# Kernel optimization log

Measured on AMD Instinct MI355X. Metric: run time of the kernel, lower is better.

Reference implementation:

```python
import jax, jax.numpy as jnp
from jax import lax
import numpy as np

N = 1024           # num_nodes
E = 32768          # edges per hop adjacency (avg degree 32)
EMB, HID, REP = 128, 64, 32
PATH_LENGTHS = (2, 3)


def _conv2d(x, w, b, pad):
    y = lax.conv_general_dilated(x, w, (1, 1), [(pad, pad), (pad, pad)],
                                 dimension_numbers=('NCHW', 'OIHW', 'NCHW'))
    return y + b[None, :, None, None]


def _tconv2d(x, w, b):
    # ConvTranspose2d(kernel=2, stride=2, pad=0) == conv with lhs_dilation=2, pad=1 (out = 2*in)
    y = lax.conv_general_dilated(x, w, (1, 1), [(1, 1), (1, 1)],
                                 lhs_dilation=(2, 2),
                                 dimension_numbers=('NCHW', 'OIHW', 'NCHW'))
    return y + b[None, :, None, None]


def _maxpool2(x):
    return lax.reduce_window(x, -jnp.inf, lax.max, (1, 1, 2, 2), (1, 1, 2, 2), 'VALID')


def _att_block(a, p):
    # ConvEncoder: conv->pool->conv->pool->tconv->tconv, relu/relu/relu/sigmoid
    h = jax.nn.relu(_conv2d(a, p[0], p[1], 1))
    h = _maxpool2(h)
    h = jax.nn.relu(_conv2d(h, p[2], p[3], 2))
    h = _maxpool2(h)
    h = jax.nn.relu(_tconv2d(h, p[4], p[5]))
    return jax.nn.sigmoid(_tconv2d(h, p[6], p[7]))


def _dense_gcn_norm(A):
    # add_remaining_self_loops(fill=1) + D^{-1/2} A D^{-1/2}; deg = row-sum (scatter_add over row)
    A = A + jnp.diag(jnp.where(jnp.diagonal(A) == 0, 1.0, 0.0).astype(A.dtype))
    deg = A.sum(axis=1)
    safe = jnp.where(deg > 0, deg, 1.0)
    dinv = jnp.where(deg > 0, lax.rsqrt(safe), 0.0)
    return dinv[:, None] * A * dinv[None, :]


def _edges_to_dense(e):
    # torch.sparse.FloatTensor(idx, ones).to_dense() sums duplicate edges
    return jnp.zeros((N, N), jnp.float32).at[e[0], e[1]].add(1.0)


def _path_transform(adjs, p):
    # adjs: [L, N, N] dense per-hop adjacencies of one meta-path
    att = _att_block(adjs[None], p)[0][:, :N, :N]
    attended = adjs * att
    M = jnp.eye(N, dtype=adjs.dtype)
    for i in range(adjs.shape[0]):  # fixed small loop over hops
        M = _dense_gcn_norm(M @ attended[i])
    return M


def _forward(x, p0, p1, w1, bias1, w2, bias2, e00, e01, e10, e11, e12):
    A0 = jnp.stack([_edges_to_dense(e00), _edges_to_dense(e01)])
    A1 = jnp.stack([_edges_to_dense(e10), _edges_to_dense(e11), _edges_to_dense(e12)])
    M0 = _path_transform(A0, p0)
    M1 = _path_transform(A1, p1)
    A = jnp.maximum(M0, M1)  # coalesce(op='max') over union; values are >= 0
    An = _dense_gcn_norm(A)  # GCNConv internal normalization (same for both layers)
    h = jax.nn.relu(An @ (x @ w1) + bias1)
    # dropout inactive (eval mode)
    return An @ (h @ w2) + bias2


def setup_inputs():
    key = jax.random.key(0)
    ks = iter(jax.random.split(key, 40))
    d = {}
    d['x'] = jax.random.normal(next(ks), (N, EMB), jnp.float32)
    d['mp0_e0'] = jax.random.randint(next(ks), (2, E), 0, N)
    d['mp0_e1'] = jax.random.randint(next(ks), (2, E), 0, N)
    d['mp1_e0'] = jax.random.randint(next(ks), (2, E), 0, N)
    d['mp1_e1'] = jax.random.randint(next(ks), (2, E), 0, N)
    d['mp1_e2'] = jax.random.randint(next(ks), (2, E), 0, N)
    for bi, L in enumerate(PATH_LENGTHS):
        pre = 'b%d_' % bi
        d[pre + 'c1w'] = jax.random.normal(next(ks), (16, L, 3, 3), jnp.float32) * 0.1
        d[pre + 'c1b'] = jnp.zeros((16,), jnp.float32)
        d[pre + 'c2w'] = jax.random.normal(next(ks), (4, 16, 3, 3), jnp.float32) * 0.1
        d[pre + 'c2b'] = jnp.zeros((4,), jnp.float32)
        d[pre + 't1w'] = jax.random.normal(next(ks), (16, 4, 2, 2), jnp.float32) * 0.1
        d[pre + 't1b'] = jnp.zeros((16,), jnp.float32)
        d[pre + 't2w'] = jax.random.normal(next(ks), (L, 16, 2, 2), jnp.float32) * 0.1
        d[pre + 't2b'] = jnp.zeros((L,), jnp.float32)
    d['w1'] = jax.random.normal(next(ks), (EMB, HID), jnp.float32) * (1.0 / np.sqrt(EMB)).astype(np.float32)
    d['bias1'] = jnp.zeros((HID,), jnp.float32)
    d['w2'] = jax.random.normal(next(ks), (HID, REP), jnp.float32) * (1.0 / np.sqrt(HID)).astype(np.float32)
    d['bias2'] = jnp.zeros((REP,), jnp.float32)
    return d


def reference(x, mp0_e0, mp0_e1, mp1_e0, mp1_e1, mp1_e2,
              b0_c1w, b0_c1b, b0_c2w, b0_c2b, b0_t1w, b0_t1b, b0_t2w, b0_t2b,
              b1_c1w, b1_c1b, b1_c2w, b1_c2b, b1_t1w, b1_t1b, b1_t2w, b1_t2b,
              w1, bias1, w2, bias2):
    p0 = (b0_c1w, b0_c1b, b0_c2w, b0_c2b, b0_t1w, b0_t1b, b0_t2w, b0_t2b)
    p1 = (b1_c1w, b1_c1b, b1_c2w, b1_c2b, b1_t1w, b1_t1b, b1_t2w, b1_t2b)
    return _forward(x, p0, p1, w1, bias1, w2, bias2,
                    mp0_e0, mp0_e1, mp1_e0, mp1_e1, mp1_e2)
```

## Files before the change

kernel.cpp:

```cpp
#include <hip/hip_runtime.h>
#include <math.h>

#define N 1024
#define NN (N*N)
#define NE 32768

#define OFF_A    ((size_t)0)
#define OFF_H10  ((size_t)(5*NN))
#define OFF_M0   ((size_t)(5*NN))
#define OFF_CSR  ((size_t)(7*NN))
#define OFF_BT   ((size_t)(9*NN))
#define OFF_M1   ((size_t)(10*NN))
#define OFF_AN   ((size_t)(11*NN))
#define OFF_H20  ((size_t)(13*NN))
#define OFF_H21  (OFF_H20 + 264196)
#define OFF_SC   (OFF_H21 + 264196)
#define SC_D0a 0
#define SC_F0a 1024
#define SC_D1a 2048
#define SC_F1a 3072
#define SC_D0b 4096
#define SC_F0b 5120
#define SC_D1b 6144
#define SC_F1b 7168
#define SC_D1c 8192
#define SC_F1c 9216
#define SC_D2  10240
#define SC_F2  11264
#define OFF_XW1  (OFF_SC + 12288)
#define OFF_HB   (OFF_XW1 + 65536)
#define OFF_HW2  (OFF_HB + 65536)

#define CSR_STRIDE 96
#define CSRF (1024 * CSR_STRIDE)
#define CSC_MAXT 80

__global__ void k_scatter5(const int* __restrict__ e0, const int* __restrict__ e1,
                           const int* __restrict__ e2, const int* __restrict__ e3,
                           const int* __restrict__ e4, float* __restrict__ A) {
  int g = blockIdx.x * 256 + threadIdx.x;
  int seg = g >> 15;
  int k = g & 32767;
  const int* e = (seg == 0) ? e0 : (seg == 1) ? e1 : (seg == 2) ? e2 : (seg == 3) ? e3 : e4;
  atomicAdd(&A[(size_t)seg * NN + (size_t)e[k] * N + e[NE + k]], 1.0f);
}

template<int L>
__device__ __forceinline__ void conv1_body(const float* __restrict__ A,
    const float* __restrict__ W, const float* __restrict__ Bn, float* __restrict__ out) {
  __shared__ float sIn[L][34][35];
  __shared__ float sW[16 * L * 9];
  __shared__ float sB[16];
  int tid = threadIdx.y * 16 + threadIdx.x;
  for (int i = tid; i < 16 * L * 9; i += 256) sW[i] = W[i];
  if (tid < 16) sB[tid] = Bn[tid];
  const int x0 = blockIdx.x * 32 - 1;
  const int y0 = blockIdx.y * 32 - 1;
  for (int idx = tid; idx < L * 34 * 34; idx += 256) {
    int l = idx / (34 * 34);
    int rem = idx - l * 34 * 34;
    int r = rem / 34, c = rem - r * 34;
    int iy = y0 + r, ix = x0 + c;
    sIn[l][r][c] = (iy >= 0 && iy < N && ix >= 0 && ix < N) ? A[(size_t)l * NN + (size_t)iy * N + ix] : 0.f;
  }
  __syncthreads();
  const int tx = threadIdx.x, ty = threadIdx.y;
  float p[L][4][4];
  #pragma unroll
  for (int l = 0; l < L; ++l)
    #pragma unroll
    for (int r = 0; r < 4; ++r)
      #pragma unroll
      for (int c = 0; c < 4; ++c)
        p[l][r][c] = sIn[l][2 * ty + r][2 * tx + c];
  const int ox = blockIdx.x * 16 + tx;
  const int oy = blockIdx.y * 16 + ty;
  for (int oc = 0; oc < 16; ++oc) {
    float wr[L * 9];
    #pragma unroll
    for (int t = 0; t < L * 9; ++t) wr[t] = sW[oc * L * 9 + t];
    float m = -1e30f;
    #pragma unroll
    for (int dy = 0; dy < 2; ++dy)
      #pragma unroll
      for (int dx = 0; dx < 2; ++dx) {
        float s = 0.f;
        #pragma unroll
        for (int l = 0; l < L; ++l)
          #pragma unroll
          for (int ky = 0; ky < 3; ++ky)
            #pragma unroll
            for (int kx = 0; kx < 3; ++kx)
              s = fmaf(p[l][dy + ky][dx + kx], wr[l * 9 + ky * 3 + kx], s);
        m = fmaxf(m, s);
      }
    out[(size_t)oc * 512 * 512 + (size_t)oy * 512 + ox] = fmaxf(m + sB[oc], 0.f);
  }
}

__global__ __launch_bounds__(256) void k_conv1_both(const float* __restrict__ Ab,
    const float* __restrict__ W0, const float* __restrict__ b0,
    const float* __restrict__ W1, const float* __restrict__ b1, float* __restrict__ H1b) {
  if (blockIdx.z == 0) conv1_body<2>(Ab, W0, b0, H1b);
  else                 conv1_body<3>(Ab + 2 * NN, W1, b1, H1b + 4 * NN);
}

__global__ __launch_bounds__(256) void k_conv2_both(const float* __restrict__ H1b,
    const float* __restrict__ W0, const float* __restrict__ b0,
    const float* __restrict__ W1, const float* __restrict__ b1,
    float* __restrict__ H2_0, float* __restrict__ H2_1) {
  const int z = blockIdx.z;
  const float* in = H1b + (size_t)z * 4 * NN;
  const float* W  = z ? W1 : W0;
  const float* Bn = z ? b1 : b0;
  float* out = z ? H2_1 : H2_0;
  __shared__ float sIn[2][4][36][37];
  __shared__ float sW[4 * 16 * 9];
  __shared__ float sB[4];
  int tid = threadIdx.y * 16 + threadIdx.x;
  for (int i = tid; i < 4 * 16 * 9; i += 256) sW[i] = W[i];
  if (tid < 4) sB[tid] = Bn[tid];
  const int x0 = blockIdx.x * 32 - 2;
  const int y0 = blockIdx.y * 32 - 2;
  const int tx = threadIdx.x, ty = threadIdx.y;

  auto stage = [&](int g, int buf) {
    for (int idx = tid; idx < 4 * 36 * 36; idx += 256) {
      int icl = idx / 1296;
      int rem = idx - icl * 1296;
      int r = rem / 36, c = rem - r * 36;
      int iy = y0 + r, ix = x0 + c;
      sIn[buf][icl][r][c] = (iy >= 0 && iy < 512 && ix >= 0 && ix < 512)
                            ? in[(size_t)(4 * g + icl) * 262144 + (size_t)iy * 512 + ix] : 0.f;
    }
  };

  float acc[4][2][2];
  #pragma unroll
  for (int oc = 0; oc < 4; ++oc)
    #pragma unroll
    for (int dy = 0; dy < 2; ++dy)
      #pragma unroll
      for (int dx = 0; dx < 2; ++dx) acc[oc][dy][dx] = 0.f;

  stage(0, 0);
  for (int g = 0; g < 4; ++g) {
    __syncthreads();
    if (g < 3) stage(g + 1, (g + 1) & 1);
    const int buf = g & 1;
    #pragma unroll
    for (int icl = 0; icl < 4; ++icl) {
      float p[4][4];
      #pragma unroll
      for (int r = 0; r < 4; ++r)
        #pragma unroll
        for (int c = 0; c < 4; ++c) p[r][c] = sIn[buf][icl][2 * ty + r][2 * tx + c];
      #pragma unroll
      for (int oc = 0; oc < 4; ++oc)
        #pragma unroll
        for (int ky = 0; ky < 3; ++ky)
          #pragma unroll
          for (int kx = 0; kx < 3; ++kx) {
            float w = sW[oc * 144 + (4 * g + icl) * 9 + ky * 3 + kx];
            #pragma unroll
            for (int dy = 0; dy < 2; ++dy)
              #pragma unroll
              for (int dx = 0; dx < 2; ++dx)
                acc[oc][dy][dx] = fmaf(p[dy + ky][dx + kx], w, acc[oc][dy][dx]);
          }
    }
  }
  const int ox = blockIdx.x * 16 + tx;
  const int oy = blockIdx.y * 16 + ty;
  if (ox < 257 && oy < 257) {
    #pragma unroll
    for (int oc = 0; oc < 4; ++oc) {
      float m = fmaxf(fmaxf(acc[oc][0][0], acc[oc][0][1]), fmaxf(acc[oc][1][0], acc[oc][1][1]));
      out[(size_t)oc * 66049 + (size_t)oy * 257 + ox] = fmaxf(m + sB[oc], 0.f);
    }
  }
}

__global__ __launch_bounds__(256) void k_tc_both(
    const float* __restrict__ H2_0, const float* __restrict__ H2_1,
    const float* __restrict__ t1w0, const float* __restrict__ t1b0,
    const float* __restrict__ t2w0, const float* __restrict__ t2b0,
    const float* __restrict__ t1w1, const float* __restrict__ t1b1,
    const float* __restrict__ t2w1, const float* __restrict__ t2b1,
    float* __restrict__ Ab) {
  const int z = blockIdx.z;
  const int L = 2 + z;
  const float* in  = z ? H2_1 : H2_0;
  const float* W1p = z ? t1w1 : t1w0;
  const float* B1p = z ? t1b1 : t1b0;
  const float* W2p = z ? t2w1 : t2w0;
  const float* B2p = z ? t2b1 : t2b0;
  float* A = Ab + (size_t)z * 2 * NN;
  __shared__ float sW1[256], sB1[16], sW2[192], sB2[3];
  int tid = threadIdx.y * 16 + threadIdx.x;
  sW1[tid] = W1p[tid];
  if (tid < 16) sB1[tid] = B1p[tid];
  for (int i = tid; i < L * 64; i += 256) sW2[i] = W2p[i];
  if (tid < L) sB2[tid] = B2p[tid];
  __syncthreads();
  const int n = blockIdx.x * 16 + threadIdx.x;
  const int m = blockIdx.y * 16 + threadIdx.y;
  const int p = m >> 1, q = n >> 1;
  const int f1y = 1 - (m & 1), f1x = 1 - (n & 1);
  float vin[4];
  #pragma unroll
  for (int ci = 0; ci < 4; ++ci) vin[ci] = in[(size_t)ci * 66049 + (size_t)p * 257 + q];
  float v[16];
  #pragma unroll
  for (int c = 0; c < 16; ++c) {
    float s = sB1[c];
    #pragma unroll
    for (int ci = 0; ci < 4; ++ci)
      s = fmaf(vin[ci], sW1[c * 16 + ci * 4 + f1y * 2 + f1x], s);
    v[c] = fmaxf(s, 0.f);
  }
  for (int l = 0; l < L; ++l) {
    #pragma unroll
    for (int dy = 0; dy < 2; ++dy)
      #pragma unroll
      for (int dx = 0; dx < 2; ++dx) {
        float s = sB2[l];
        #pragma unroll
        for (int c = 0; c < 16; ++c)
          s = fmaf(v[c], sW2[l * 64 + c * 4 + (1 - dy) * 2 + (1 - dx)], s);
        float sg = 1.f / (1.f + expf(-s));
        size_t idx = (size_t)l * NN + (size_t)(2 * m + dy) * N + (2 * n + dx);
        A[idx] *= sg;
      }
  }
}

__global__ __launch_bounds__(256) void k_extract(const float* __restrict__ Ab,
    int* __restrict__ gcol, float* __restrict__ gval, int* __restrict__ gcnt,
    int* __restrict__ crowT, float* __restrict__ cvalT, int* __restrict__ ccnt,
    float* __restrict__ D0a, float* __restrict__ F0a,
    float* __restrict__ D1a, float* __restrict__ F1a) {
  const int row = blockIdx.x;
  const int y = blockIdx.y;
  const float* base = Ab + (size_t)y * NN + (size_t)row * N;
  __shared__ int cnt;
  __shared__ float sdiag;
  __shared__ float red[4];
  if (threadIdx.x == 0) cnt = 0;
  __syncthreads();
  const int j4 = threadIdx.x;
  float4 v = ((const float4*)base)[j4];
  if (j4 == (row >> 2)) sdiag = ((const float*)&v)[row & 3];
  if (y == 4) {
    #pragma unroll
    for (int t = 0; t < 4; ++t) {
      float x = ((const float*)&v)[t];
      if (x != 0.f) {
        int j = 4 * j4 + t;
        int p = atomicAdd(&ccnt[j], 1);
        if (p < CSC_MAXT) { crowT[p * 1024 + j] = row; cvalT[p * 1024 + j] = x; }
      }
    }
    return;
  }
  const size_t rb = ((size_t)y * 1024 + row) * CSR_STRIDE;
  #pragma unroll
  for (int t = 0; t < 4; ++t) {
    float x = ((const float*)&v)[t];
    if (x != 0.f) {
      int p = atomicAdd(&cnt, 1);
      if (p < CSR_STRIDE) { gcol[rb + p] = 4 * j4 + t; gval[rb + p] = x; }
    }
  }
  float s = v.x + v.y + v.z + v.w;
  #pragma unroll
  for (int o = 32; o > 0; o >>= 1) s += __shfl_down(s, o, 64);
  if ((threadIdx.x & 63) == 0) red[threadIdx.x >> 6] = s;
  __syncthreads();
  if (threadIdx.x == 0) {
    gcnt[(size_t)y * 1024 + row] = (cnt < CSR_STRIDE) ? cnt : CSR_STRIDE;
    if (y == 0 || y == 2) {
      float tot = red[0] + red[1] + red[2] + red[3];
      float fl = (sdiag == 0.f) ? 1.f : 0.f;
      float deg = tot + fl;
      float* D = (y == 0) ? D0a : D1a;
      float* F = (y == 0) ? F0a : F1a;
      D[row] = (deg > 0.f) ? (1.f / sqrtf(deg)) : 0.f;
      F[row] = fl;
    }
  }
}

__global__ __launch_bounds__(256) void k_spmm(
    const int* __restrict__ gcol, const float* __restrict__ gval, const int* __restrict__ gcnt,
    const float* __restrict__ D0a, const float* __restrict__ F0a,
    const float* __restrict__ D1a, const float* __restrict__ F1a,
    float* __restrict__ M0, float* __restrict__ BT,
    float* __restrict__ D0b, float* __restrict__ F0b,
    float* __restrict__ D1b, float* __restrict__ F1b) {
  const int row = blockIdx.x;
  const int y = blockIdx.y;
  const int lm = y * 2, rm = y * 2 + 1;
  const float* Da = y ? D1a : D0a;
  const float* Fa = y ? F1a : F0a;
  __shared__ __align__(16) float acc[1024];
  __shared__ int lcol[112];
  __shared__ float lw[112];
  __shared__ int lrc[112];
  __shared__ int cl;
  __shared__ float red[4];
  __shared__ float sdiag;
  ((float4*)acc)[threadIdx.x] = make_float4(0.f, 0.f, 0.f, 0.f);
  const float di = Da[row];
  const int cnt_l = gcnt[(size_t)lm * 1024 + row];
  const size_t lb = ((size_t)lm * 1024 + row) * CSR_STRIDE;
  if (threadIdx.x < cnt_l) {
    int k = gcol[lb + threadIdx.x];
    lcol[threadIdx.x] = k;
    lw[threadIdx.x] = di * gval[lb + threadIdx.x] * Da[k];
    lrc[threadIdx.x] = gcnt[(size_t)rm * 1024 + k];
  }
  if (threadIdx.x == 0) {
    int c = cnt_l;
    if (Fa[row] != 0.f) {
      lcol[c] = row; lw[c] = di * di; lrc[c] = gcnt[(size_t)rm * 1024 + row]; ++c;
    }
    cl = c;
  }
  __syncthreads();
  const int sub = threadIdx.x >> 5, lane = threadIdx.x & 31;
  const int cle = cl;
  for (int e = sub; e < cle; e += 8) {
    const int k = lcol[e];
    const float w = lw[e];
    const int rc = lrc[e];
    const size_t rbv = ((size_t)rm * 1024 + k) * CSR_STRIDE;
    for (int t = lane; t < rc; t += 32)
      atomicAdd(&acc[gcol[rbv + t]], w * gval[rbv + t]);
  }
  __syncthreads();
  float4 o = ((const float4*)acc)[threadIdx.x];
  float* C = y ? BT : M0;
  ((float4*)(C + (size_t)row * N))[threadIdx.x] = o;
  if (threadIdx.x == (row >> 2)) sdiag = ((const float*)&o)[row & 3];
  float s = o.x + o.y + o.z + o.w;
  #pragma unroll
  for (int off = 32; off > 0; off >>= 1) s += __shfl_down(s, off, 64);
  if ((threadIdx.x & 63) == 0) red[threadIdx.x >> 6] = s;
  __syncthreads();
  if (threadIdx.x == 0) {
    float tot = red[0] + red[1] + red[2] + red[3];
    float fl = (sdiag == 0.f) ? 1.f : 0.f;
    float deg = tot + fl;
    float* D = y ? D1b : D0b;
    float* F = y ? F1b : F0b;
    D[row] = (deg > 0.f) ? (1.f / sqrtf(deg)) : 0.f;
    F[row] = fl;
  }
}

__global__ __launch_bounds__(256) void k_spmm2(const float* __restrict__ BT,
    const float* __restrict__ D1b, const float* __restrict__ F1b,
    const int* __restrict__ crowT, const float* __restrict__ cvalT, const int* __restrict__ ccnt,
    float* __restrict__ M1, float* __restrict__ D1c, float* __restrict__ F1c) {
  const int row = blockIdx.x;
  __shared__ __align__(16) float bt[1024];
  __shared__ float red[4];
  __shared__ float sdiag;
  const int tid = threadIdx.x;
  {
    float4 b = ((const float4*)(BT + (size_t)row * N))[tid];
    float4 d = ((const float4*)D1b)[tid];
    ((float4*)bt)[tid] = make_float4(b.x * d.x, b.y * d.y, b.z * d.z, b.w * d.w);
  }
  __syncthreads();
  if (tid == 0) bt[row] += F1b[row] * D1b[row];
  __syncthreads();
  const int j0 = tid << 2;
  int4 cn = *(const int4*)&ccnt[j0];
  cn.x = min(cn.x, CSC_MAXT); cn.y = min(cn.y, CSC_MAXT);
  cn.z = min(cn.z, CSC_MAXT); cn.w = min(cn.w, CSC_MAXT);
  const int tmax = max(max(cn.x, cn.y), max(cn.z, cn.w));
  float4 o = make_float4(0.f, 0.f, 0.f, 0.f);
  for (int t = 0; t < tmax; ++t) {
    const int4   r = *(const int4*)&crowT[t * 1024 + j0];
    const float4 v = *(const float4*)&cvalT[t * 1024 + j0];
    if (t < cn.x) o.x = fmaf(bt[r.x], v.x, o.x);
    if (t < cn.y) o.y = fmaf(bt[r.y], v.y, o.y);
    if (t < cn.z) o.z = fmaf(bt[r.z], v.z, o.z);
    if (t < cn.w) o.w = fmaf(bt[r.w], v.w, o.w);
  }
  const float dr = D1b[row];
  o.x *= dr; o.y *= dr; o.z *= dr; o.w *= dr;
  ((float4*)(M1 + (size_t)row * N))[tid] = o;
  if (tid == (row >> 2)) sdiag = ((const float*)&o)[row & 3];
  float s = o.x + o.y + o.z + o.w;
  #pragma unroll
  for (int off = 32; off > 0; off >>= 1) s += __shfl_down(s, off, 64);
  if ((tid & 63) == 0) red[tid >> 6] = s;
  __syncthreads();
  if (tid == 0) {
    float tot = red[0] + red[1] + red[2] + red[3];
    float fl = (sdiag == 0.f) ? 1.f : 0.f;
    float deg = tot + fl;
    D1c[row] = (deg > 0.f) ? (1.f / sqrtf(deg)) : 0.f;
    F1c[row] = fl;
  }
}

__global__ __launch_bounds__(256) void k_maxdeg(const float* __restrict__ M0,
    const float* __restrict__ d0, const float* __restrict__ f0,
    const float* __restrict__ M1, const float* __restrict__ d1, const float* __restrict__ f1,
    float* __restrict__ Aout, float* __restrict__ dinv2, float* __restrict__ dflg2) {
  const int row = blockIdx.x;
  const int j4 = threadIdx.x;
  const float r0 = d0[row], r1 = d1[row];
  const float fl0 = f0[row], fl1 = f1[row];
  float4 a = ((const float4*)(M0 + (size_t)row * N))[j4];
  float4 b = ((const float4*)(M1 + (size_t)row * N))[j4];
  const float4 c0 = ((const float4*)d0)[j4];
  const float4 c1 = ((const float4*)d1)[j4];
  int d = row - 4 * j4;
  if ((unsigned)d < 4u) { ((float*)&a)[d] += fl0; ((float*)&b)[d] += fl1; }
  float4 o;
  o.x = fmaxf(a.x * r0 * c0.x, b.x * r1 * c1.x);
  o.y = fmaxf(a.y * r0 * c0.y, b.y * r1 * c1.y);
  o.z = fmaxf(a.z * r0 * c0.z, b.z * r1 * c1.z);
  o.w = fmaxf(a.w * r0 * c0.w, b.w * r1 * c1.w);
  ((float4*)(Aout + (size_t)row * N))[j4] = o;
  __shared__ float sdiag;
  if ((unsigned)d < 4u) sdiag = ((float*)&o)[d];
  float s = o.x + o.y + o.z + o.w;
  #pragma unroll
  for (int off = 32; off > 0; off >>= 1) s += __shfl_down(s, off, 64);
  __shared__ float red[4];
  if ((threadIdx.x & 63) == 0) red[threadIdx.x >> 6] = s;
  __syncthreads();
  if (threadIdx.x == 0) {
    float tot = red[0] + red[1] + red[2] + red[3];
    float fl = (sdiag == 0.0f) ? 1.0f : 0.0f;
    float deg = tot + fl;
    dinv2[row] = (deg > 0.0f) ? (1.0f / sqrtf(deg)) : 0.0f;
    dflg2[row] = fl;
  }
}

template<int K, int NCOL, bool BIAS, bool RELU>
__global__ void k_mm_small(const float* __restrict__ A, const float* __restrict__ B,
                           const float* __restrict__ bias, float* __restrict__ out) {
  const int j = threadIdx.x;
  const int i = blockIdx.x * blockDim.y + threadIdx.y;
  const float* ar = A + (size_t)i * K;
  float acc = 0.f;
  #pragma unroll 8
  for (int k = 0; k < K; ++k) acc = fmaf(ar[k], B[(size_t)k * NCOL + j], acc);
  if (BIAS) acc += bias[j];
  if (RELU) acc = fmaxf(acc, 0.f);
  out[(size_t)i * NCOL + j] = acc;
}

template<int NCOL, bool RELU>
__global__ void k_an_mm(const float* __restrict__ BT, const float* __restrict__ dinv,
                        const float* __restrict__ dflg, const float* __restrict__ Bm,
                        const float* __restrict__ bias, float* __restrict__ out) {
  const int j = threadIdx.x;
  const int i = blockIdx.x * blockDim.y + threadIdx.y;
  const float di = dinv[i];
  const float* ar = BT + (size_t)i * N;
  float acc = 0.f;
  for (int k = 0; k < N; k += 4) {
    float4 a4 = *(const float4*)&ar[k];
    float4 d4 = *(const float4*)&dinv[k];
    acc = fmaf(a4.x * d4.x, Bm[(size_t)(k + 0) * NCOL + j], acc);
    acc = fmaf(a4.y * d4.y, Bm[(size_t)(k + 1) * NCOL + j], acc);
    acc = fmaf(a4.z * d4.z, Bm[(size_t)(k + 2) * NCOL + j], acc);
    acc = fmaf(a4.w * d4.w, Bm[(size_t)(k + 3) * NCOL + j], acc);
  }
  acc = fmaf(dflg[i] * dinv[i], Bm[(size_t)i * NCOL + j], acc);
  acc = fmaf(di, acc, bias[j]);
  if (RELU) acc = fmaxf(acc, 0.f);
  out[(size_t)i * NCOL + j] = acc;
}

extern "C" void kernel_launch(void* const* d_in, const int* in_sizes, int n_in,
                              void* d_out, int out_size, void* d_ws, size_t ws_size,
                              hipStream_t stream) {
  const float* x     = (const float*)d_in[0];
  const float* w1    = (const float*)d_in[22];
  const float* bias1 = (const float*)d_in[23];
  const float* w2    = (const float*)d_in[24];
  const float* bias2 = (const float*)d_in[25];
  float* out = (float*)d_out;
  float* ws  = (float*)d_ws;

  float* A    = ws + OFF_A;
  float* H1   = ws + OFF_H10;
  float* M0   = ws + OFF_M0;
  float* BT   = ws + OFF_BT;
  float* M1   = ws + OFF_M1;
  float* AN   = ws + OFF_AN;
  float* H2_0 = ws + OFF_H20;
  float* H2_1 = ws + OFF_H21;
  int*   gcol  = (int*)(ws + OFF_CSR);
  float* gval  = ws + OFF_CSR + (size_t)4 * CSRF;
  int*   gcnt  = (int*)(ws + OFF_CSR + (size_t)8 * CSRF);
  int*   crowT = (int*)(ws + OFF_CSR + (size_t)8 * CSRF + 4096);
  float* cvalT = ws + OFF_CSR + (size_t)8 * CSRF + 4096 + CSC_MAXT * 1024;
  int*   ccnt  = (int*)(ws + OFF_CSR + (size_t)8 * CSRF + 4096 + (size_t)2 * CSC_MAXT * 1024);
  float* SC   = ws + OFF_SC;
  float *D0a = SC + SC_D0a, *F0a = SC + SC_F0a, *D1a = SC + SC_D1a, *F1a = SC + SC_F1a;
  float *D0b = SC + SC_D0b, *F0b = SC + SC_F0b, *D1b = SC + SC_D1b, *F1b = SC + SC_F1b;
  float *D1c = SC + SC_D1c, *F1c = SC + SC_F1c, *D2 = SC + SC_D2, *F2 = SC + SC_F2;
  float* XW1 = ws + OFF_XW1;
  float* HB  = ws + OFF_HB;
  float* HW2 = ws + OFF_HW2;

  hipMemsetAsync(A, 0, (size_t)5 * NN * sizeof(float), stream);

  dim3 b256(256), b16(16, 16);
  k_mm_small<128, 64, false, false><<<256, dim3(64, 4), 0, stream>>>(x, w1, nullptr, XW1);

  k_scatter5<<<640, b256, 0, stream>>>((const int*)d_in[1], (const int*)d_in[2],
                                       (const int*)d_in[3], (const int*)d_in[4],
                                       (const int*)d_in[5], A);

  k_conv1_both<<<dim3(32, 32, 2), b16, 0, stream>>>(A,
      (const float*)d_in[6], (const float*)d_in[7],
      (const float*)d_in[14], (const float*)d_in[15], H1);
  k_conv2_both<<<dim3(17, 17, 2), b16, 0, stream>>>(H1,
      (const float*)d_in[8], (const float*)d_in[9],
      (const float*)d_in[16], (const float*)d_in[17], H2_0, H2_1);
  k_tc_both<<<dim3(32, 32, 2), b16, 0, stream>>>(H2_0, H2_1,
      (const float*)d_in[10], (const float*)d_in[11],
      (const float*)d_in[12], (const float*)d_in[13],
      (const float*)d_in[18], (const float*)d_in[19],
      (const float*)d_in[20], (const float*)d_in[21], A);

  hipMemsetAsync(ccnt, 0, 1024 * sizeof(int), stream);

  k_extract<<<dim3(1024, 5), b256, 0, stream>>>(A, gcol, gval, gcnt,
      crowT, cvalT, ccnt, D0a, F0a, D1a, F1a);

  k_spmm<<<dim3(1024, 2), b256, 0, stream>>>(gcol, gval, gcnt,
      D0a, F0a, D1a, F1a, M0, BT, D0b, F0b, D1b, F1b);

  k_spmm2<<<1024, b256, 0, stream>>>(BT, D1b, F1b, crowT, cvalT, ccnt, M1, D1c, F1c);

  k_maxdeg<<<1024, b256, 0, stream>>>(M0, D0b, F0b, M1, D1c, F1c, AN, D2, F2);

  k_an_mm<64, true><<<256, dim3(64, 4), 0, stream>>>(AN, D2, F2, XW1, bias1, HB);
  k_mm_small<64, 32, false, false><<<128, dim3(32, 8), 0, stream>>>(HB, w2, nullptr, HW2);
  k_an_mm<32, false><<<128, dim3(32, 8), 0, stream>>>(AN, D2, F2, HW2, bias2, out);
}
```

Before: 380.0 us.

## Restructure CSC SpMM to process eight rows per block with column-split grid

The second sparse multiply now gives each block eight output rows and a 256-column slice, so every CSC entry load (row index and value) is reused across eight rows instead of being reread per row. The eight BT rows are staged in shared memory with a padded stride of 9. Row degrees are now reduced across column slices with atomics into an accumulator that k_extract zeroes, and a new small k_fin kernel computes the rsqrt normalisation and self-loop flags. This adds a kernel launch, uses 36KB of shared memory per block, and makes the degree float sums order-dependent.

Result: slower. 392.1 us (+3.2%).

```diff
diff --git a/kernel.cpp b/kernel.cpp
--- a/kernel.cpp
+++ b/kernel.cpp
@@ -27,7 +27,9 @@
 #define SC_F1c 9216
 #define SC_D2  10240
 #define SC_F2  11264
-#define OFF_XW1  (OFF_SC + 12288)
+#define SC_DEG 12288
+#define SC_DGV 13312
+#define OFF_XW1  (OFF_SC + 14336)
 #define OFF_HB   (OFF_XW1 + 65536)
 #define OFF_HW2  (OFF_HB + 65536)
 
@@ -238,6 +240,7 @@
 __global__ __launch_bounds__(256) void k_extract(const float* __restrict__ Ab,
     int* __restrict__ gcol, float* __restrict__ gval, int* __restrict__ gcnt,
     int* __restrict__ crowT, float* __restrict__ cvalT, int* __restrict__ ccnt,
+    float* __restrict__ DEGACC,
     float* __restrict__ D0a, float* __restrict__ F0a,
     float* __restrict__ D1a, float* __restrict__ F1a) {
   const int row = blockIdx.x;
@@ -252,6 +255,7 @@
   float4 v = ((const float4*)base)[j4];
   if (j4 == (row >> 2)) sdiag = ((const float*)&v)[row & 3];
   if (y == 4) {
+    if (threadIdx.x == 0) DEGACC[row] = 0.f;
     #pragma unroll
     for (int t = 0; t < 4; ++t) {
       float x = ((const float*)&v)[t];
@@ -362,50 +366,65 @@
 __global__ __launch_bounds__(256) void k_spmm2(const float* __restrict__ BT,
     const float* __restrict__ D1b, const float* __restrict__ F1b,
     const int* __restrict__ crowT, const float* __restrict__ cvalT, const int* __restrict__ ccnt,
-    float* __restrict__ M1, float* __restrict__ D1c, float* __restrict__ F1c) {
-  const int row = blockIdx.x;
-  __shared__ __align__(16) float bt[1024];
-  __shared__ float red[4];
-  __shared__ float sdiag;
+    float* __restrict__ M1, float* __restrict__ DEGACC, float* __restrict__ DIAGV) {
+  const int g0 = blockIdx.x << 3;
+  const int j  = (blockIdx.y << 8) + threadIdx.x;
+  __shared__ float bt[1024 * 9];
+  __shared__ float wsum[4][8];
   const int tid = threadIdx.x;
-  {
-    float4 b = ((const float4*)(BT + (size_t)row * N))[tid];
-    float4 d = ((const float4*)D1b)[tid];
-    ((float4*)bt)[tid] = make_float4(b.x * d.x, b.y * d.y, b.z * d.z, b.w * d.w);
-  }
-  __syncthreads();
-  if (tid == 0) bt[row] += F1b[row] * D1b[row];
-  __syncthreads();
-  const int j0 = tid << 2;
-  int4 cn = *(const int4*)&ccnt[j0];
-  cn.x = min(cn.x, CSC_MAXT); cn.y = min(cn.y, CSC_MAXT);
-  cn.z = min(cn.z, CSC_MAXT); cn.w = min(cn.w, CSC_MAXT);
-  const int tmax = max(max(cn.x, cn.y), max(cn.z, cn.w));
-  float4 o = make_float4(0.f, 0.f, 0.f, 0.f);
-  for (int t = 0; t < tmax; ++t) {
-    const int4   r = *(const int4*)&crowT[t * 1024 + j0];
-    const float4 v = *(const float4*)&cvalT[t * 1024 + j0];
-    if (t < cn.x) o.x = fmaf(bt[r.x], v.x, o.x);
-    if (t < cn.y) o.y = fmaf(bt[r.y], v.y, o.y);
-    if (t < cn.z) o.z = fmaf(bt[r.z], v.z, o.z);
-    if (t < cn.w) o.w = fmaf(bt[r.w], v.w, o.w);
-  }
-  const float dr = D1b[row];
-  o.x *= dr; o.y *= dr; o.z *= dr; o.w *= dr;
-  ((float4*)(M1 + (size_t)row * N))[tid] = o;
-  if (tid == (row >> 2)) sdiag = ((const float*)&o)[row & 3];
-  float s = o.x + o.y + o.z + o.w;
-  #pragma unroll
-  for (int off = 32; off > 0; off >>= 1) s += __shfl_down(s, off, 64);
-  if ((tid & 63) == 0) red[tid >> 6] = s;
-  __syncthreads();
-  if (tid == 0) {
-    float tot = red[0] + red[1] + red[2] + red[3];
-    float fl = (sdiag == 0.f) ? 1.f : 0.f;
-    float deg = tot + fl;
-    D1c[row] = (deg > 0.f) ? (1.f / sqrtf(deg)) : 0.f;
-    F1c[row] = fl;
-  }
+  for (int kq = 0; kq < 4; ++kq) {
+    const int k = (kq << 8) + tid;
+    const float dv = D1b[k];
+    #pragma unroll
+    for (int row = 0; row < 8; ++row)
+      bt[k * 9 + row] = BT[(size_t)(g0 + row) * N + k] * dv;
+  }
+  __syncthreads();
+  if (tid < 8) {
+    const int gr = g0 + tid;
+    bt[gr * 9 + tid] += F1b[gr] * D1b[gr];
+  }
+  __syncthreads();
+  int cn = ccnt[j];
+  cn = min(cn, CSC_MAXT);
+  float o[8];
+  #pragma unroll
+  for (int row = 0; row < 8; ++row) o[row] = 0.f;
+  for (int t = 0; t < cn; ++t) {
+    const int   r = crowT[t * 1024 + j];
+    const float v = cvalT[t * 1024 + j];
+    const int rb = r * 9;
+    #pragma unroll
+    for (int row = 0; row < 8; ++row)
+      o[row] = fmaf(bt[rb + row], v, o[row]);
+  }
+  #pragma unroll
+  for (int row = 0; row < 8; ++row) o[row] *= D1b[g0 + row];
+  #pragma unroll
+  for (int row = 0; row < 8; ++row)
+    M1[(size_t)(g0 + row) * N + j] = o[row];
+  if ((unsigned)(j - g0) < 8u) DIAGV[j] = o[j - g0];
+  #pragma unroll
+  for (int row = 0; row < 8; ++row) {
+    float s = o[row];
+    #pragma unroll
+    for (int off = 32; off > 0; off >>= 1) s += __shfl_down(s, off, 64);
+    if ((tid & 63) == 0) wsum[tid >> 6][row] = s;
+  }
+  __syncthreads();
+  if (tid < 8) {
+    float p = wsum[0][tid] + wsum[1][tid] + wsum[2][tid] + wsum[3][tid];
+    atomicAdd(&DEGACC[g0 + tid], p);
+  }
+}
+
+__global__ void k_fin(const float* __restrict__ DEGACC, const float* __restrict__ DIAGV,
+                      float* __restrict__ D1c, float* __restrict__ F1c) {
+  const int row = blockIdx.x * 256 + threadIdx.x;
+  const float fl = (DIAGV[row] == 0.f) ? 1.f : 0.f;
+  const float deg = DEGACC[row] + fl;
+  D1c[row] = (deg > 0.f) ? (1.f / sqrtf(deg)) : 0.f;
+  F1c[row] = fl;
 }
 
 __global__ __launch_bounds__(256) void k_maxdeg(const float* __restrict__ M0,
@@ -511,6 +530,7 @@
   float *D0a = SC + SC_D0a, *F0a = SC + SC_F0a, *D1a = SC + SC_D1a, *F1a = SC + SC_F1a;
   float *D0b = SC + SC_D0b, *F0b = SC + SC_F0b, *D1b = SC + SC_D1b, *F1b = SC + SC_F1b;
   float *D1c = SC + SC_D1c, *F1c = SC + SC_F1c, *D2 = SC + SC_D2, *F2 = SC + SC_F2;
+  float *DEGACC = SC + SC_DEG, *DIAGV = SC + SC_DGV;
   float* XW1 = ws + OFF_XW1;
   float* HB  = ws + OFF_HB;
   float* HW2 = ws + OFF_HW2;
@@ -539,12 +559,14 @@
   hipMemsetAsync(ccnt, 0, 1024 * sizeof(int), stream);
 
   k_extract<<<dim3(1024, 5), b256, 0, stream>>>(A, gcol, gval, gcnt,
-      crowT, cvalT, ccnt, D0a, F0a, D1a, F1a);
+      crowT, cvalT, ccnt, DEGACC, D0a, F0a, D1a, F1a);
 
   k_spmm<<<dim3(1024, 2), b256, 0, stream>>>(gcol, gval, gcnt,
       D0a, F0a, D1a, F1a, M0, BT, D0b, F0b, D1b, F1b);
 
-  k_spmm2<<<1024, b256, 0, stream>>>(BT, D1b, F1b, crowT, cvalT, ccnt, M1, D1c, F1c);
+  k_spmm2<<<dim3(128, 4), b256, 0, stream>>>(BT, D1b, F1b, crowT, cvalT, ccnt,
+                                             M1, DEGACC, DIAGV);
+  k_fin<<<4, b256, 0, stream>>>(DEGACC, DIAGV, D1c, F1c);
 
   k_maxdeg<<<1024, b256, 0, stream>>>(M0, D0b, F0b, M1, D1c, F1c, AN, D2, F2);
 
```
